# Kernel optimization log

Hardware: AMD Instinct MI355X
Metric: run time of the kernel (lower is better)

Reference implementation:

```python
import jax, jax.numpy as jnp
import numpy as np


def _gaussian_orthogonal_random_matrix(nb_rows, nb_cols, seed=0):
    rng = np.random.default_rng(seed)
    blocks = []
    n_full = nb_rows // nb_cols
    for _ in range(n_full):
        q, _ = np.linalg.qr(rng.standard_normal((nb_cols, nb_cols)).astype(np.float64))
        blocks.append(q.T)
    rem = nb_rows - n_full * nb_cols
    if rem > 0:
        q, _ = np.linalg.qr(rng.standard_normal((nb_cols, nb_cols)).astype(np.float64))
        blocks.append(q.T[:rem])
    final = np.concatenate(blocks, axis=0)
    # scaling == 0: row multipliers are norms of gaussian rows
    multiplier = np.linalg.norm(rng.standard_normal((nb_rows, nb_cols)), axis=1)
    return (multiplier[:, None] * final).astype(np.float32)


def setup_inputs() -> dict:
    key = jax.random.key(0)
    kq, kk, kv = jax.random.split(key, 3)
    B, H, N, D = 4, 16, 4096, 64
    M = 256  # nb_features
    return {
        "q": jax.random.normal(kq, (B, H, N, D), dtype=jnp.float32),
        "k": jax.random.normal(kk, (B, H, N, D), dtype=jnp.float32),
        "v": jax.random.normal(kv, (B, H, N, D), dtype=jnp.float32),
        "projection_matrix": jnp.asarray(_gaussian_orthogonal_random_matrix(M, D)),
    }


def _softmax_kernel(data, proj, is_query, eps=1e-4):
    # data: [b,h,n,d], proj: [m,d]
    d = data.shape[-1]
    m = proj.shape[0]
    data_normalizer = d ** -0.25
    ratio = m ** -0.5
    data_dash = jnp.einsum('bhnd,md->bhnm', data_normalizer * data, proj)
    diag_data = jnp.sum(data * data, axis=-1, keepdims=True) * 0.5 * (data_normalizer ** 2)
    if is_query:
        mx = jnp.max(data_dash, axis=-1, keepdims=True)
    else:
        mx = jnp.max(data_dash, axis=(-2, -1), keepdims=True)
    mx = jax.lax.stop_gradient(mx)
    return ratio * (jnp.exp(data_dash - diag_data - mx) + eps)


def _linear_attention(q, k, v):
    # q,k: [b,h,n,m]; v: [b,h,n,e]
    k_cumsum = k.sum(axis=-2)                              # [b,h,m]
    d_inv = 1.0 / jnp.einsum('bhnm,bhm->bhn', q, k_cumsum)  # [b,h,n]
    context = jnp.einsum('bhnm,bhne->bhme', k, v)          # [b,h,m,e]
    return jnp.einsum('bhme,bhnm,bhn->bhne', context, q, d_inv)


def reference(q, k, v, projection_matrix):
    qp = _softmax_kernel(q, projection_matrix, is_query=True)
    kp = _softmax_kernel(k, projection_matrix, is_query=False)
    return _linear_attention(qp, kp, v)
```

## Files before the change

### kernel.cpp

```cpp
#include <hip/hip_runtime.h>
#include <math.h>

#define NSEQ  4096
#define DDIM  64
#define GH    64
#define NORMC 0.35355339059327373f
#define EPSC  1e-4f

typedef __bf16 bf16x8 __attribute__((ext_vector_type(8)));
typedef unsigned short u16x8 __attribute__((ext_vector_type(8)));
typedef unsigned short u16x4 __attribute__((ext_vector_type(4)));
typedef float f32x4 __attribute__((ext_vector_type(4)));

__device__ __forceinline__ unsigned enc_f(float f) {
    unsigned b = __float_as_uint(f);
    return (b & 0x80000000u) ? ~b : (b | 0x80000000u);
}
__device__ __forceinline__ float dec_f(unsigned u) {
    return (u & 0x80000000u) ? __uint_as_float(u & 0x7FFFFFFFu) : __uint_as_float(~u);
}
__device__ __forceinline__ void split_hl(float f, unsigned short& h, unsigned short& l) {
    unsigned u = __float_as_uint(f);
    unsigned hb = u & 0xffff0000u;
    h = (unsigned short)(hb >> 16);
    l = (unsigned short)(__float_as_uint(f - __uint_as_float(hb)) >> 16);
}
__device__ __forceinline__ unsigned short rne16(float f) {
    return (unsigned short)((__float_as_uint(f) + 0x8000u) >> 16);
}
__device__ __forceinline__ bf16x8 ldfrag(const unsigned short* p) {
    return __builtin_bit_cast(bf16x8, *(const u16x8*)p);
}
__device__ __forceinline__ f32x4 zero4() { f32x4 z = {0.f, 0.f, 0.f, 0.f}; return z; }
__device__ __forceinline__ f32x4 mfma3(bf16x8 ah, bf16x8 al, bf16x8 bh, bf16x8 bl, f32x4 c) {
    c = __builtin_amdgcn_mfma_f32_16x16x32_bf16(ah, bh, c, 0, 0, 0);
    c = __builtin_amdgcn_mfma_f32_16x16x32_bf16(ah, bl, c, 0, 0, 0);
    c = __builtin_amdgcn_mfma_f32_16x16x32_bf16(al, bh, c, 0, 0, 0);
    return c;
}

template<int NSLICE>
__global__ __launch_bounds__(256, 2)
void kernA(const float* __restrict__ kk, const float* __restrict__ vv,
           const float* __restrict__ proj, float* __restrict__ Apart,
           float* __restrict__ Aspart, float* __restrict__ Svpart,
           unsigned* __restrict__ mxk)
{
    const int slices = (NSLICE == 1) ? 16 : NSLICE;
    const int bx    = blockIdx.x;
    const int slice = bx & (slices - 1);
    const int mh    = bx / slices;
    const int g     = blockIdx.y;
    const int t     = threadIdx.x;
    const int lane  = t & 63;
    const int wq    = t >> 6;
    const int li    = lane & 15;
    const int lg    = lane >> 4;

    __shared__ __align__(16) unsigned short ARENA[12288];
    __shared__ float diag[2][32];
    __shared__ float svred[4][64];
    __shared__ float mxred[4];

    bf16x8 pfh[2][2], pfl[2][2];
#pragma unroll
    for (int u = 0; u < 2; u++)
#pragma unroll
    for (int s = 0; s < 2; s++) {
        const float* pr = proj + (size_t)(mh * 128 + wq * 32 + u * 16 + li) * DDIM + s * 32 + lg * 8;
        u16x8 hh, ll;
#pragma unroll
        for (int j = 0; j < 8; j++) {
            unsigned short h, l;
            split_hl(NORMC * pr[j], h, l);
            hh[j] = h; ll[j] = l;
        }
        pfh[u][s] = __builtin_bit_cast(bf16x8, hh);
        pfl[u][s] = __builtin_bit_cast(bf16x8, ll);
    }

    f32x4 cacc[4][2];
#pragma unroll
    for (int a = 0; a < 4; a++)
#pragma unroll
    for (int b = 0; b < 2; b++) cacc[a][b] = zero4();
    float as_loc[2] = {0.f, 0.f};
    float sv8[8] = {0.f,0.f,0.f,0.f,0.f,0.f,0.f,0.f};
    float mloc = -1e30f;

    const int stg_n = t >> 3;
    const int stg_c = t & 7;
    const int rows_per = NSEQ / slices;
    const int r_begin = slice * rows_per;
    const int vks = ((stg_n >> 2) & 3) * 8 + (stg_n >> 4) * 4 + (stg_n & 3);

    float4 ka0, ka1, va0, va1;
    auto load_tile = [&](int r0) {
        const float4* kb = (const float4*)(kk + ((size_t)g * NSEQ + r0 + stg_n) * DDIM + stg_c * 8);
        ka0 = kb[0]; ka1 = kb[1];
        const float4* vb = (const float4*)(vv + ((size_t)g * NSEQ + r0 + stg_n) * DDIM + stg_c * 8);
        va0 = vb[0]; va1 = vb[1];
    };
    auto stage_tile = [&](int b) {
        unsigned short* Khi  = ARENA + b * 6144;
        unsigned short* Klo  = Khi + 2048;
        unsigned short* Vthi = Khi + 4096;
        float ke[8] = {ka0.x,ka0.y,ka0.z,ka0.w,ka1.x,ka1.y,ka1.z,ka1.w};
        float sq = 0.f;
#pragma unroll
        for (int j = 0; j < 8; j++) sq += ke[j] * ke[j];
        sq += __shfl_xor(sq, 1); sq += __shfl_xor(sq, 2); sq += __shfl_xor(sq, 4);
        if (stg_c == 0) diag[b][stg_n] = 0.0625f * sq;
        u16x8 h8, l8;
#pragma unroll
        for (int j = 0; j < 8; j++) {
            unsigned short h, l;
            split_hl(ke[j], h, l);
            h8[j] = h; l8[j] = l;
        }
        int idx = stg_n * 64 + (stg_c ^ (stg_n & 7)) * 8;
        *(u16x8*)&Khi[idx] = h8;
        *(u16x8*)&Klo[idx] = l8;
        float ve[8] = {va0.x,va0.y,va0.z,va0.w,va1.x,va1.y,va1.z,va1.w};
#pragma unroll
        for (int j = 0; j < 8; j++) {
            sv8[j] += ve[j];
            int e = stg_c * 8 + j;
            int slot = vks ^ (((e >> 1) & 3) << 3);
            Vthi[e * 32 + slot] = rne16(ve[j]);
        }
    };

    load_tile(r_begin);
    stage_tile(0);
    __syncthreads();
    int cur = 0;
    const int NT = rows_per / 32;
    for (int it = 0; it < NT; ++it) {
        if (it + 1 < NT) load_tile(r_begin + (it + 1) * 32);
        const unsigned short* Khi  = ARENA + cur * 6144;
        const unsigned short* Klo  = Khi + 2048;
        const unsigned short* Vthi = Khi + 4096;
        f32x4 dacc[2][2];
#pragma unroll
        for (int tt = 0; tt < 2; tt++)
#pragma unroll
        for (int u = 0; u < 2; u++) dacc[tt][u] = zero4();
#pragma unroll
        for (int tt = 0; tt < 2; tt++)
#pragma unroll
        for (int s = 0; s < 2; s++) {
            int idx = (tt * 16 + li) * 64 + ((s * 4 + lg) ^ (li & 7)) * 8;
            bf16x8 ah = ldfrag(&Khi[idx]);
            bf16x8 al = ldfrag(&Klo[idx]);
#pragma unroll
            for (int u = 0; u < 2; u++) dacc[tt][u] = mfma3(ah, al, pfh[u][s], pfl[u][s], dacc[tt][u]);
        }
        u16x8 whh[2];
#pragma unroll
        for (int tt = 0; tt < 2; tt++)
#pragma unroll
        for (int u = 0; u < 2; u++)
#pragma unroll
        for (int r = 0; r < 4; r++) {
            float dash = dacc[tt][u][r];
            mloc = fmaxf(mloc, dash);
            float w = __expf(dash - diag[cur][tt * 16 + lg * 4 + r]);
            unsigned short hb = rne16(w);
            whh[u][tt * 4 + r] = hb;
            as_loc[u] += __uint_as_float((unsigned)hb << 16);
        }
        bf16x8 avh[4];
#pragma unroll
        for (int u2 = 0; u2 < 4; u2++) {
            int row = u2 * 16 + li;
            int slot = (lg ^ ((li >> 1) & 3)) * 8;
            avh[u2] = ldfrag(&Vthi[row * 32 + slot]);
        }
#pragma unroll
        for (int u = 0; u < 2; u++) {
            bf16x8 b = __builtin_bit_cast(bf16x8, whh[u]);
#pragma unroll
            for (int u2 = 0; u2 < 4; u2++)
                cacc[u2][u] = __builtin_amdgcn_mfma_f32_16x16x32_bf16(avh[u2], b, cacc[u2][u], 0, 0, 0);
        }
        if (it + 1 < NT) stage_tile(cur ^ 1);
        __syncthreads();
        cur ^= 1;
    }

#pragma unroll
    for (int j = 0; j < 8; j++) {
        float s = sv8[j];
        s += __shfl_xor(s, 8); s += __shfl_xor(s, 16); s += __shfl_xor(s, 32);
        sv8[j] = s;
    }
    if (lane < 8) {
#pragma unroll
        for (int j = 0; j < 8; j++) svred[wq][lane * 8 + j] = sv8[j];
    }
    float mm = mloc;
#pragma unroll
    for (int off = 32; off >= 1; off >>= 1) mm = fmaxf(mm, __shfl_xor(mm, off));
    if (lane == 0) mxred[wq] = mm;
#pragma unroll
    for (int u = 0; u < 2; u++) {
        float a = as_loc[u];
        a += __shfl_xor(a, 16); a += __shfl_xor(a, 32);
        as_loc[u] = a;
    }
    __syncthreads();
    if (t == 0) {
        float m4 = fmaxf(fmaxf(mxred[0], mxred[1]), fmaxf(mxred[2], mxred[3]));
        atomicMax(mxk + g, enc_f(m4));
    }
    if (t < 64 && mh == 0) {
        float s = svred[0][t] + svred[1][t] + svred[2][t] + svred[3][t];
        if (NSLICE == 1) atomicAdd(&Svpart[(size_t)g * 64 + t], s);
        else             Svpart[((size_t)g * NSLICE + slice) * 64 + t] = s;
    }
    if (lane < 16) {
#pragma unroll
        for (int u = 0; u < 2; u++) {
            int m = mh * 128 + wq * 32 + u * 16 + lane;
            if (NSLICE == 1) atomicAdd(&Aspart[(size_t)g * 256 + m], as_loc[u]);
            else             Aspart[((size_t)g * NSLICE + slice) * 256 + m] = as_loc[u];
        }
    }
    float* tb = (float*)ARENA + wq * 1024;
    float* Ad = (NSLICE == 1) ? (Apart + (size_t)g * 16384)
                              : (Apart + ((size_t)g * NSLICE + slice) * 16384);
    for (int u = 0; u < 2; u++) {
#pragma unroll
        for (int u2 = 0; u2 < 4; u2++)
#pragma unroll
        for (int r = 0; r < 4; r++)
            tb[li * 64 + ((((u2 << 2) | lg) ^ (li & 7)) << 2) + r] = cacc[u2][u][r];
#pragma unroll
        for (int j = 0; j < 4; j++) {
            int row16 = j * 4 + lg;
            int swz = li ^ (row16 & 7);
            f32x4 val = *(const f32x4*)&tb[row16 * 64 + swz * 4];
            float* dst = Ad + (mh * 128 + wq * 32 + u * 16) * 64 + j * 256 + lane * 4;
            if (NSLICE == 1) {
                atomicAdd(dst + 0, val[0]); atomicAdd(dst + 1, val[1]);
                atomicAdd(dst + 2, val[2]); atomicAdd(dst + 3, val[3]);
            } else {
                *(f32x4*)dst = val;
            }
        }
    }
}

__global__ __launch_bounds__(256)
void kernB(const float* __restrict__ Apart, const float* __restrict__ Aspart,
           const float* __restrict__ Svpart, const unsigned* __restrict__ mxk,
           unsigned short* __restrict__ ctxTh, float* __restrict__ ksum, int nslice)
{
    const int b = blockIdx.x;
    const int g = blockIdx.y;
    const int t = threadIdx.x;
    __shared__ float svh[64];
    __shared__ float TB[16][68];
    float emx = __expf(-dec_f(mxk[g]));
    if (t < 64) {
        float s = 0.f;
        for (int sb = 0; sb < nslice; sb++) s += Svpart[((size_t)g * nslice + sb) * 64 + t];
        svh[t] = s;
    }
    if (b == 0) {
        float as_s = 0.f;
        for (int sb = 0; sb < nslice; sb++) as_s += Aspart[((size_t)g * nslice + sb) * 256 + t];
        ksum[(size_t)g * 256 + t] = emx * as_s + EPSC * (float)NSEQ;
    }
    __syncthreads();
    const int mi = t >> 6, e = t & 63;
#pragma unroll
    for (int p = 0; p < 4; p++) {
        int ml = p * 4 + mi;
        int m  = b * 16 + ml;
        float s = 0.f;
        for (int sb = 0; sb < nslice; sb++)
            s += Apart[((size_t)g * nslice + sb) * 16384 + m * 64 + e];
        TB[ml][e] = emx * s + EPSC * svh[e];
    }
    __syncthreads();
    const int er = t >> 2, mj = (t & 3) * 4;
    u16x4 h4;
#pragma unroll
    for (int i = 0; i < 4; i++) h4[i] = rne16(TB[mj + i][er]);
    size_t base = (size_t)g * 16384 + (size_t)er * 256 + b * 16 + mj;
    *(u16x4*)&ctxTh[base] = h4;
}

__global__ __launch_bounds__(256, 2)
void kernC(const float* __restrict__ qq, const float* __restrict__ proj,
           const unsigned short* __restrict__ ctxTh,
           const float* __restrict__ ksum, float* __restrict__ outp)
{
    const int slice = blockIdx.x;
    const int g     = blockIdx.y;
    const int t     = threadIdx.x;
    const int lane  = t & 63;
    const int wq    = t >> 6;
    const int li    = lane & 15;
    const int lg    = lane >> 4;

    __shared__ __align__(16) unsigned short QAR[2][4096];
    __shared__ __align__(16) unsigned short qph[8192];
    __shared__ float diag[2][32];
    __shared__ float rmax4[4][32];
    __shared__ float denp[4][32];

    bf16x8 pfh[4][2], pfl[4][2];
#pragma unroll
    for (int u = 0; u < 4; u++)
#pragma unroll
    for (int s = 0; s < 2; s++) {
        const float* pr = proj + (size_t)(wq * 64 + u * 16 + li) * DDIM + s * 32 + lg * 8;
        u16x8 hh, ll;
#pragma unroll
        for (int j = 0; j < 8; j++) {
            unsigned short h, l;
            split_hl(NORMC * pr[j], h, l);
            hh[j] = h; ll[j] = l;
        }
        pfh[u][s] = __builtin_bit_cast(bf16x8, hh);
        pfl[u][s] = __builtin_bit_cast(bf16x8, ll);
    }
    float ksm[4];
#pragma unroll
    for (int u = 0; u < 4; u++) ksm[u] = ksum[(size_t)g * 256 + wq * 64 + u * 16 + li];

    const unsigned short* axbh = ctxTh + (size_t)g * 16384 + (size_t)(wq * 16 + li) * 256 + lg * 8;

    const int stg_n = t >> 3;
    const int stg_c = t & 7;
    const int r_begin = slice * (NSEQ / 16);

    float4 qa0, qa1;
    auto load_tile = [&](int r0) {
        const float4* qb = (const float4*)(qq + ((size_t)g * NSEQ + r0 + stg_n) * DDIM + stg_c * 8);
        qa0 = qb[0]; qa1 = qb[1];
    };
    auto stage_tile = [&](int b) {
        float qe[8] = {qa0.x,qa0.y,qa0.z,qa0.w,qa1.x,qa1.y,qa1.z,qa1.w};
        float sq = 0.f;
#pragma unroll
        for (int j = 0; j < 8; j++) sq += qe[j] * qe[j];
        sq += __shfl_xor(sq, 1); sq += __shfl_xor(sq, 2); sq += __shfl_xor(sq, 4);
        if (stg_c == 0) diag[b][stg_n] = 0.0625f * sq;
        u16x8 h8, l8;
#pragma unroll
        for (int j = 0; j < 8; j++) {
            unsigned short h, l;
            split_hl(qe[j], h, l);
            h8[j] = h; l8[j] = l;
        }
        int idx = stg_n * 64 + (stg_c ^ (stg_n & 7)) * 8;
        *(u16x8*)&QAR[b][idx] = h8;
        *(u16x8*)&QAR[b][2048 + idx] = l8;
    };

    load_tile(r_begin);
    stage_tile(0);
    __syncthreads();
    int cur = 0;
    for (int it = 0; it < 8; ++it) {
        if (it + 1 < 8) load_tile(r_begin + (it + 1) * 32);
        f32x4 dacc[2][4];
#pragma unroll
        for (int tt = 0; tt < 2; tt++)
#pragma unroll
        for (int u = 0; u < 4; u++) dacc[tt][u] = zero4();
#pragma unroll
        for (int tt = 0; tt < 2; tt++)
#pragma unroll
        for (int s = 0; s < 2; s++) {
            int idx = (tt * 16 + li) * 64 + ((s * 4 + lg) ^ (li & 7)) * 8;
            bf16x8 ah = ldfrag(&QAR[cur][idx]);
            bf16x8 al = ldfrag(&QAR[cur][2048 + idx]);
#pragma unroll
            for (int u = 0; u < 4; u++) dacc[tt][u] = mfma3(ah, al, pfh[u][s], pfl[u][s], dacc[tt][u]);
        }
#pragma unroll
        for (int tt = 0; tt < 2; tt++)
#pragma unroll
        for (int r = 0; r < 4; r++) {
            float v = fmaxf(fmaxf(dacc[tt][0][r], dacc[tt][1][r]),
                            fmaxf(dacc[tt][2][r], dacc[tt][3][r]));
            v = fmaxf(v, __shfl_xor(v, 1));
            v = fmaxf(v, __shfl_xor(v, 2));
            v = fmaxf(v, __shfl_xor(v, 4));
            v = fmaxf(v, __shfl_xor(v, 8));
            if (li == 0) rmax4[wq][tt * 16 + lg * 4 + r] = v;
        }
        __syncthreads();
        float dl[2][4] = {{0.f,0.f,0.f,0.f},{0.f,0.f,0.f,0.f}};
#pragma unroll
        for (int tt = 0; tt < 2; tt++) {
            float cb[4];
#pragma unroll
            for (int r = 0; r < 4; r++) {
                int n = tt * 16 + lg * 4 + r;
                cb[r] = diag[cur][n] + fmaxf(fmaxf(rmax4[0][n], rmax4[1][n]),
                                             fmaxf(rmax4[2][n], rmax4[3][n]));
            }
#pragma unroll
            for (int u = 0; u < 4; u++)
#pragma unroll
            for (int r = 0; r < 4; r++) {
                float qp = __expf(dacc[tt][u][r] - cb[r]) + EPSC;
                unsigned short hb = rne16(qp);
                dl[tt][r] += __uint_as_float((unsigned)hb << 16) * ksm[u];
                int n = tt * 16 + lg * 4 + r;
                int mg = wq * 64 + u * 16 + li;
                qph[n * 256 + (((mg >> 3) ^ (n & 7)) << 3) + (mg & 7)] = hb;
            }
        }
#pragma unroll
        for (int tt = 0; tt < 2; tt++)
#pragma unroll
        for (int r = 0; r < 4; r++) {
            float v = dl[tt][r];
            v += __shfl_xor(v, 1); v += __shfl_xor(v, 2);
            v += __shfl_xor(v, 4); v += __shfl_xor(v, 8);
            if (li == 0) denp[wq][tt * 16 + lg * 4 + r] = v;
        }
        if (it + 1 < 8) stage_tile(cur ^ 1);
        __syncthreads();
        bf16x8 axh[8];
#pragma unroll
        for (int mc = 0; mc < 8; mc++)
            axh[mc] = __builtin_bit_cast(bf16x8, *(const u16x8*)(axbh + mc * 32));
        f32x4 oacc[2] = {zero4(), zero4()};
#pragma unroll
        for (int tt = 0; tt < 2; tt++) {
            int n = tt * 16 + li;
#pragma unroll
            for (int mc = 0; mc < 8; mc++) {
                bf16x8 b = ldfrag(&qph[n * 256 + (((mc * 4 + lg) ^ (li & 7)) << 3)]);
                oacc[tt] = __builtin_amdgcn_mfma_f32_16x16x32_bf16(axh[mc], b, oacc[tt], 0, 0, 0);
            }
        }
#pragma unroll
        for (int tt = 0; tt < 2; tt++) {
            int n = tt * 16 + li;
            float den = denp[0][n] + denp[1][n] + denp[2][n] + denp[3][n];
            float dinv = 1.0f / den;
            f32x4 o;
            o[0] = oacc[tt][0] * dinv; o[1] = oacc[tt][1] * dinv;
            o[2] = oacc[tt][2] * dinv; o[3] = oacc[tt][3] * dinv;
            float* op = outp + ((size_t)g * NSEQ + r_begin + it * 32 + n) * DDIM + wq * 16 + lg * 4;
            *(f32x4*)op = o;
        }
        cur ^= 1;
    }
}

extern "C" void kernel_launch(void* const* d_in, const int* in_sizes, int n_in,
                              void* d_out, int out_size, void* d_ws, size_t ws_size,
                              hipStream_t stream)
{
    const float* q    = (const float*)d_in[0];
    const float* k    = (const float*)d_in[1];
    const float* v    = (const float*)d_in[2];
    const float* proj = (const float*)d_in[3];
    float* outp = (float*)d_out;

    size_t per_ns = (size_t)GH * 16384 + (size_t)GH * 256 + (size_t)GH * 64;
    size_t fixed  = (size_t)GH * 16384 + (size_t)GH * 256;
    size_t need8  = 256 + 4 * (8 * per_ns + fixed);
    int ns = (ws_size >= need8) ? 8 : 1;

    unsigned* mxk = (unsigned*)d_ws;
    float* Apart  = (float*)((char*)d_ws + 256);
    float* Aspart = Apart  + (size_t)GH * ns * 16384;
    float* Svpart = Aspart + (size_t)GH * ns * 256;
    float* ctx    = Svpart + (size_t)GH * ns * 64;
    float* ksum   = ctx    + (size_t)GH * 16384;

    unsigned short* ctxTh = (unsigned short*)ctx;

    if (ns == 8) {
        hipMemsetAsync(d_ws, 0, 256, stream);
        kernA<8><<<dim3(16, GH), 256, 0, stream>>>(k, v, proj, Apart, Aspart, Svpart, mxk);
    } else {
        hipMemsetAsync(d_ws, 0, 256 + 4 * per_ns, stream);
        kernA<1><<<dim3(32, GH), 256, 0, stream>>>(k, v, proj, Apart, Aspart, Svpart, mxk);
    }
    kernB<<<dim3(16, GH), 256, 0, stream>>>(Apart, Aspart, Svpart, mxk, ctxTh, ksum, ns);
    kernC<<<dim3(16, GH), 256, 0, stream>>>(q, proj, ctxTh, ksum, outp);
}
```

Before: 188.7 us.

## Fuse context reduction into kernA via last-block counter; enlarge kernC tile to 64 rows

Removes the separate kernB launch. Each kernA block now increments a per-head counter after a threadfence, and the last-arriving block reduces the slice partials into ksum and the bf16 transposed context. That saves a launch and a kernel boundary, but the whole per-head reduction is serialised onto one block. kernC now processes 64 query rows per iteration with a single staging buffer over 4 iterations instead of 32 rows over 8. This gives more MFMA work per barrier at the cost of more shared memory and registers, which may lower occupancy.

```diff
diff --git a/kernel.cpp b/kernel.cpp
--- a/kernel.cpp
+++ b/kernel.cpp
@@ -44,7 +44,8 @@
 void kernA(const float* __restrict__ kk, const float* __restrict__ vv,
            const float* __restrict__ proj, float* __restrict__ Apart,
            float* __restrict__ Aspart, float* __restrict__ Svpart,
-           unsigned* __restrict__ mxk)
+           unsigned* __restrict__ mxk, unsigned* __restrict__ cnt,
+           unsigned short* __restrict__ ctxTh, float* __restrict__ ksum)
 {
     const int slices = (NSLICE == 1) ? 16 : NSLICE;
     const int bx    = blockIdx.x;
@@ -61,6 +62,7 @@
     __shared__ float diag[2][32];
     __shared__ float svred[4][64];
     __shared__ float mxred[4];
+    __shared__ unsigned rank_s;
 
     bf16x8 pfh[2][2], pfl[2][2];
 #pragma unroll
@@ -227,70 +229,73 @@
             else             Aspart[((size_t)g * NSLICE + slice) * 256 + m] = as_loc[u];
         }
     }
-    float* tb = (float*)ARENA + wq * 1024;
-    float* Ad = (NSLICE == 1) ? (Apart + (size_t)g * 16384)
-                              : (Apart + ((size_t)g * NSLICE + slice) * 16384);
-    for (int u = 0; u < 2; u++) {
-#pragma unroll
-        for (int u2 = 0; u2 < 4; u2++)
-#pragma unroll
-        for (int r = 0; r < 4; r++)
-            tb[li * 64 + ((((u2 << 2) | lg) ^ (li & 7)) << 2) + r] = cacc[u2][u][r];
-#pragma unroll
-        for (int j = 0; j < 4; j++) {
-            int row16 = j * 4 + lg;
-            int swz = li ^ (row16 & 7);
-            f32x4 val = *(const f32x4*)&tb[row16 * 64 + swz * 4];
-            float* dst = Ad + (mh * 128 + wq * 32 + u * 16) * 64 + j * 256 + lane * 4;
-            if (NSLICE == 1) {
-                atomicAdd(dst + 0, val[0]); atomicAdd(dst + 1, val[1]);
-                atomicAdd(dst + 2, val[2]); atomicAdd(dst + 3, val[3]);
-            } else {
-                *(f32x4*)dst = val;
+    {
+        float* tb = (float*)ARENA + wq * 1024;
+        float* Ad = (NSLICE == 1) ? (Apart + (size_t)g * 16384)
+                                  : (Apart + ((size_t)g * NSLICE + slice) * 16384);
+        for (int u = 0; u < 2; u++) {
+#pragma unroll
+            for (int u2 = 0; u2 < 4; u2++)
+#pragma unroll
+            for (int r = 0; r < 4; r++)
+                tb[li * 64 + ((((u2 << 2) | lg) ^ (li & 7)) << 2) + r] = cacc[u2][u][r];
+#pragma unroll
+            for (int j = 0; j < 4; j++) {
+                int row16 = j * 4 + lg;
+                int swz = li ^ (row16 & 7);
+                f32x4 val = *(const f32x4*)&tb[row16 * 64 + swz * 4];
+                float* dst = Ad + (mh * 128 + wq * 32 + u * 16) * 64 + j * 256 + lane * 4;
+                if (NSLICE == 1) {
+                    atomicAdd(dst + 0, val[0]); atomicAdd(dst + 1, val[1]);
+                    atomicAdd(dst + 2, val[2]); atomicAdd(dst + 3, val[3]);
+                } else {
+                    *(f32x4*)dst = val;
+                }
             }
         }
     }
-}
-
-__global__ __launch_bounds__(256)
-void kernB(const float* __restrict__ Apart, const float* __restrict__ Aspart,
-           const float* __restrict__ Svpart, const unsigned* __restrict__ mxk,
-           unsigned short* __restrict__ ctxTh, float* __restrict__ ksum, int nslice)
-{
-    const int b = blockIdx.x;
-    const int g = blockIdx.y;
-    const int t = threadIdx.x;
-    __shared__ float svh[64];
-    __shared__ float TB[16][68];
-    float emx = __expf(-dec_f(mxk[g]));
-    if (t < 64) {
-        float s = 0.f;
-        for (int sb = 0; sb < nslice; sb++) s += Svpart[((size_t)g * nslice + sb) * 64 + t];
-        svh[t] = s;
-    }
-    if (b == 0) {
-        float as_s = 0.f;
-        for (int sb = 0; sb < nslice; sb++) as_s += Aspart[((size_t)g * nslice + sb) * 256 + t];
-        ksum[(size_t)g * 256 + t] = emx * as_s + EPSC * (float)NSEQ;
-    }
+
+    __threadfence();
+    if (t == 0) rank_s = atomicAdd(&cnt[g], 1u);
     __syncthreads();
-    const int mi = t >> 6, e = t & 63;
-#pragma unroll
-    for (int p = 0; p < 4; p++) {
-        int ml = p * 4 + mi;
-        int m  = b * 16 + ml;
-        float s = 0.f;
-        for (int sb = 0; sb < nslice; sb++)
-            s += Apart[((size_t)g * nslice + sb) * 16384 + m * 64 + e];
-        TB[ml][e] = emx * s + EPSC * svh[e];
-    }
-    __syncthreads();
-    const int er = t >> 2, mj = (t & 3) * 4;
-    u16x4 h4;
-#pragma unroll
-    for (int i = 0; i < 4; i++) h4[i] = rne16(TB[mj + i][er]);
-    size_t base = (size_t)g * 16384 + (size_t)er * 256 + b * 16 + mj;
-    *(u16x4*)&ctxTh[base] = h4;
+    const unsigned lastrank = (NSLICE == 1) ? 31u : 15u;
+    if (rank_s == lastrank) {
+        __threadfence();
+        const int nsl = (NSLICE == 1) ? 1 : NSLICE;
+        float emx = __expf(-dec_f(mxk[g]));
+        float* svh = &svred[0][0];
+        if (t < 64) {
+            float s = 0.f;
+            for (int sb = 0; sb < nsl; sb++) s += Svpart[((size_t)g * nsl + sb) * 64 + t];
+            svh[t] = s;
+        }
+        {
+            float as_s = 0.f;
+            for (int sb = 0; sb < nsl; sb++) as_s += Aspart[((size_t)g * nsl + sb) * 256 + t];
+            ksum[(size_t)g * 256 + t] = emx * as_s + EPSC * (float)NSEQ;
+        }
+        __syncthreads();
+        float* TB = (float*)ARENA;
+        const int mi = t >> 6, e = t & 63;
+        const int er = t >> 2, mj = (t & 3) * 4;
+        for (int b = 0; b < 16; b++) {
+#pragma unroll
+            for (int p = 0; p < 4; p++) {
+                int ml = p * 4 + mi;
+                int m  = b * 16 + ml;
+                float s = 0.f;
+                for (int sb = 0; sb < nsl; sb++)
+                    s += Apart[((size_t)g * nsl + sb) * 16384 + m * 64 + e];
+                TB[ml * 68 + e] = emx * s + EPSC * svh[e];
+            }
+            __syncthreads();
+            u16x4 h4;
+#pragma unroll
+            for (int i = 0; i < 4; i++) h4[i] = rne16(TB[(mj + i) * 68 + er]);
+            *(u16x4*)&ctxTh[(size_t)g * 16384 + (size_t)er * 256 + b * 16 + mj] = h4;
+            __syncthreads();
+        }
+    }
 }
 
 __global__ __launch_bounds__(256, 2)
@@ -306,11 +311,11 @@
     const int li    = lane & 15;
     const int lg    = lane >> 4;
 
-    __shared__ __align__(16) unsigned short QAR[2][4096];
-    __shared__ __align__(16) unsigned short qph[8192];
-    __shared__ float diag[2][32];
-    __shared__ float rmax4[4][32];
-    __shared__ float denp[4][32];
+    __shared__ __align__(16) unsigned short QAR[8192];
+    __shared__ __align__(16) unsigned short qph[16384];
+    __shared__ float diag[2][64];
+    __shared__ float rmax4[4][64];
+    __shared__ float denp[4][64];
 
     bf16x8 pfh[4][2], pfl[4][2];
 #pragma unroll
@@ -336,55 +341,62 @@
 
     const int stg_n = t >> 3;
     const int stg_c = t & 7;
-    const int r_begin = slice * (NSEQ / 16);
-
-    float4 qa0, qa1;
+    const int r_begin = slice * 256;
+
+    float4 qa[2][2];
     auto load_tile = [&](int r0) {
-        const float4* qb = (const float4*)(qq + ((size_t)g * NSEQ + r0 + stg_n) * DDIM + stg_c * 8);
-        qa0 = qb[0]; qa1 = qb[1];
+#pragma unroll
+        for (int h = 0; h < 2; h++) {
+            const float4* qb = (const float4*)(qq + ((size_t)g * NSEQ + r0 + stg_n + h * 32) * DDIM + stg_c * 8);
+            qa[h][0] = qb[0]; qa[h][1] = qb[1];
+        }
     };
-    auto stage_tile = [&](int b) {
-        float qe[8] = {qa0.x,qa0.y,qa0.z,qa0.w,qa1.x,qa1.y,qa1.z,qa1.w};
-        float sq = 0.f;
-#pragma unroll
-        for (int j = 0; j < 8; j++) sq += qe[j] * qe[j];
-        sq += __shfl_xor(sq, 1); sq += __shfl_xor(sq, 2); sq += __shfl_xor(sq, 4);
-        if (stg_c == 0) diag[b][stg_n] = 0.0625f * sq;
-        u16x8 h8, l8;
-#pragma unroll
-        for (int j = 0; j < 8; j++) {
-            unsigned short h, l;
-            split_hl(qe[j], h, l);
-            h8[j] = h; l8[j] = l;
-        }
-        int idx = stg_n * 64 + (stg_c ^ (stg_n & 7)) * 8;
-        *(u16x8*)&QAR[b][idx] = h8;
-        *(u16x8*)&QAR[b][2048 + idx] = l8;
+    auto stage_tile = [&](int par) {
+#pragma unroll
+        for (int h = 0; h < 2; h++) {
+            int row = stg_n + h * 32;
+            float qe[8] = {qa[h][0].x,qa[h][0].y,qa[h][0].z,qa[h][0].w,
+                           qa[h][1].x,qa[h][1].y,qa[h][1].z,qa[h][1].w};
+            float sq = 0.f;
+#pragma unroll
+            for (int j = 0; j < 8; j++) sq += qe[j] * qe[j];
+            sq += __shfl_xor(sq, 1); sq += __shfl_xor(sq, 2); sq += __shfl_xor(sq, 4);
+            if (stg_c == 0) diag[par][row] = 0.0625f * sq;
+            u16x8 h8, l8;
+#pragma unroll
+            for (int j = 0; j < 8; j++) {
+                unsigned short h, l;
+                split_hl(qe[j], h, l);
+                h8[j] = h; l8[j] = l;
+            }
+            int idx = row * 64 + (stg_c ^ (row & 7)) * 8;
+            *(u16x8*)&QAR[idx] = h8;
+            *(u16x8*)&QAR[4096 + idx] = l8;
+        }
     };
 
     load_tile(r_begin);
     stage_tile(0);
     __syncthreads();
-    int cur = 0;
-    for (int it = 0; it < 8; ++it) {
-        if (it + 1 < 8) load_tile(r_begin + (it + 1) * 32);
-        f32x4 dacc[2][4];
-#pragma unroll
-        for (int tt = 0; tt < 2; tt++)
+    for (int it = 0; it < 4; ++it) {
+        if (it + 1 < 4) load_tile(r_begin + (it + 1) * 64);
+        f32x4 dacc[4][4];
+#pragma unroll
+        for (int tt = 0; tt < 4; tt++)
 #pragma unroll
         for (int u = 0; u < 4; u++) dacc[tt][u] = zero4();
 #pragma unroll
-        for (int tt = 0; tt < 2; tt++)
+        for (int tt = 0; tt < 4; tt++)
 #pragma unroll
         for (int s = 0; s < 2; s++) {
             int idx = (tt * 16 + li) * 64 + ((s * 4 + lg) ^ (li & 7)) * 8;
-            bf16x8 ah = ldfrag(&QAR[cur][idx]);
-            bf16x8 al = ldfrag(&QAR[cur][2048 + idx]);
+            bf16x8 ah = ldfrag(&QAR[idx]);
+            bf16x8 al = ldfrag(&QAR[4096 + idx]);
 #pragma unroll
             for (int u = 0; u < 4; u++) dacc[tt][u] = mfma3(ah, al, pfh[u][s], pfl[u][s], dacc[tt][u]);
         }
 #pragma unroll
-        for (int tt = 0; tt < 2; tt++)
+        for (int tt = 0; tt < 4; tt++)
 #pragma unroll
         for (int r = 0; r < 4; r++) {
             float v = fmaxf(fmaxf(dacc[tt][0][r], dacc[tt][1][r]),
@@ -396,15 +408,19 @@
             if (li == 0) rmax4[wq][tt * 16 + lg * 4 + r] = v;
         }
         __syncthreads();
-        float dl[2][4] = {{0.f,0.f,0.f,0.f},{0.f,0.f,0.f,0.f}};
-#pragma unroll
-        for (int tt = 0; tt < 2; tt++) {
+        float dl[4][4];
+#pragma unroll
+        for (int tt = 0; tt < 4; tt++)
+#pragma unroll
+        for (int r = 0; r < 4; r++) dl[tt][r] = 0.f;
+#pragma unroll
+        for (int tt = 0; tt < 4; tt++) {
             float cb[4];
 #pragma unroll
             for (int r = 0; r < 4; r++) {
                 int n = tt * 16 + lg * 4 + r;
-                cb[r] = diag[cur][n] + fmaxf(fmaxf(rmax4[0][n], rmax4[1][n]),
-                                             fmaxf(rmax4[2][n], rmax4[3][n]));
+                cb[r] = diag[it & 1][n] + fmaxf(fmaxf(rmax4[0][n], rmax4[1][n]),
+                                                fmaxf(rmax4[2][n], rmax4[3][n]));
             }
 #pragma unroll
             for (int u = 0; u < 4; u++)
@@ -419,7 +435,7 @@
             }
         }
 #pragma unroll
-        for (int tt = 0; tt < 2; tt++)
+        for (int tt = 0; tt < 4; tt++)
 #pragma unroll
         for (int r = 0; r < 4; r++) {
             float v = dl[tt][r];
@@ -427,34 +443,33 @@
             v += __shfl_xor(v, 4); v += __shfl_xor(v, 8);
             if (li == 0) denp[wq][tt * 16 + lg * 4 + r] = v;
         }
-        if (it + 1 < 8) stage_tile(cur ^ 1);
+        if (it + 1 < 4) stage_tile((it + 1) & 1);
         __syncthreads();
         bf16x8 axh[8];
 #pragma unroll
         for (int mc = 0; mc < 8; mc++)
             axh[mc] = __builtin_bit_cast(bf16x8, *(const u16x8*)(axbh + mc * 32));
-        f32x4 oacc[2] = {zero4(), zero4()};
-#pragma unroll
-        for (int tt = 0; tt < 2; tt++) {
+        f32x4 oacc[4] = {zero4(), zero4(), zero4(), zero4()};
+#pragma unroll
+        for (int tt = 0; tt < 4; tt++) {
             int n = tt * 16 + li;
 #pragma unroll
             for (int mc = 0; mc < 8; mc++) {
-                bf16x8 b = ldfrag(&qph[n * 256 + (((mc * 4 + lg) ^ (li & 7)) << 3)]);
+                bf16x8 b = ldfrag(&qph[n * 256 + (((mc * 4 + lg) ^ (n & 7)) << 3)]);
                 oacc[tt] = __builtin_amdgcn_mfma_f32_16x16x32_bf16(axh[mc], b, oacc[tt], 0, 0, 0);
             }
         }
 #pragma unroll
-        for (int tt = 0; tt < 2; tt++) {
+        for (int tt = 0; tt < 4; tt++) {
             int n = tt * 16 + li;
             float den = denp[0][n] + denp[1][n] + denp[2][n] + denp[3][n];
             float dinv = 1.0f / den;
             f32x4 o;
             o[0] = oacc[tt][0] * dinv; o[1] = oacc[tt][1] * dinv;
             o[2] = oacc[tt][2] * dinv; o[3] = oacc[tt][3] * dinv;
-            float* op = outp + ((size_t)g * NSEQ + r_begin + it * 32 + n) * DDIM + wq * 16 + lg * 4;
+            float* op = outp + ((size_t)g * NSEQ + r_begin + it * 64 + n) * DDIM + wq * 16 + lg * 4;
             *(f32x4*)op = o;
         }
-        cur ^= 1;
     }
 }
 
@@ -470,11 +485,12 @@
 
     size_t per_ns = (size_t)GH * 16384 + (size_t)GH * 256 + (size_t)GH * 64;
     size_t fixed  = (size_t)GH * 16384 + (size_t)GH * 256;
-    size_t need8  = 256 + 4 * (8 * per_ns + fixed);
+    size_t need8  = 512 + 4 * (8 * per_ns + fixed);
     int ns = (ws_size >= need8) ? 8 : 1;
 
     unsigned* mxk = (unsigned*)d_ws;
-    float* Apart  = (float*)((char*)d_ws + 256);
+    unsigned* cnt = (unsigned*)((char*)d_ws + 256);
+    float* Apart  = (float*)((char*)d_ws + 512);
     float* Aspart = Apart  + (size_t)GH * ns * 16384;
     float* Svpart = Aspart + (size_t)GH * ns * 256;
     float* ctx    = Svpart + (size_t)GH * ns * 64;
@@ -483,12 +499,13 @@
     unsigned short* ctxTh = (unsigned short*)ctx;
 
     if (ns == 8) {
-        hipMemsetAsync(d_ws, 0, 256, stream);
-        kernA<8><<<dim3(16, GH), 256, 0, stream>>>(k, v, proj, Apart, Aspart, Svpart, mxk);
+        hipMemsetAsync(d_ws, 0, 512, stream);
+        kernA<8><<<dim3(16, GH), 256, 0, stream>>>(k, v, proj, Apart, Aspart, Svpart,
+                                                   mxk, cnt, ctxTh, ksum);
     } else {
-        hipMemsetAsync(d_ws, 0, 256 + 4 * per_ns, stream);
-        kernA<1><<<dim3(32, GH), 256, 0, stream>>>(k, v, proj, Apart, Aspart, Svpart, mxk);
-    }
-    kernB<<<dim3(16, GH), 256, 0, stream>>>(Apart, Aspart, Svpart, mxk, ctxTh, ksum, ns);
+        hipMemsetAsync(d_ws, 0, 512 + 4 * per_ns, stream);
+        kernA<1><<<dim3(32, GH), 256, 0, stream>>>(k, v, proj, Apart, Aspart, Svpart,
+                                                   mxk, cnt, ctxTh, ksum);
+    }
     kernC<<<dim3(16, GH), 256, 0, stream>>>(q, proj, ctxTh, ksum, outp);
 }
```

Measured after the change: 447.9 us. 137% more time.
